# Optimization experiments

Hardware: AMD Instinct MI355X
Metric: run time of the kernel (lower is better)

Reference implementation:

```python
import jax, jax.numpy as jnp
import numpy as np

# static config (levels=4, CDA=False branch -> self_attn_4, scale=4, f=False)
SHAPES = [(80, 80), (40, 40), (20, 20), (10, 10)]
D = 256; NH = 8; NL = 4; NP = 4; DFF = 1024; DH = D // NH
L = sum(h * w for h, w in SHAPES)  # 8500
B = 1


def layer_norm(x, g, b, eps=1e-5):
    m = jnp.mean(x, axis=-1, keepdims=True)
    v = jnp.mean((x - m) ** 2, axis=-1, keepdims=True)
    return (x - m) * jax.lax.rsqrt(v + eps) * g + b


def ms_deform_attn_core(value, loc, attn):
    # value: [B, L, NH, DH]; loc: [B, Lq, NH, NL, NP, 2] in [0,1]; attn: [B, Lq, NH, NL, NP]
    Bq, Lq = loc.shape[0], loc.shape[1]
    out = jnp.zeros((Bq, NH, Lq, DH), value.dtype)
    start = 0
    for lvl, (Hl, Wl) in enumerate(SHAPES):
        v = value[:, start:start + Hl * Wl]          # [B, HW, NH, DH]
        start += Hl * Wl
        v = v.transpose(0, 2, 1, 3)                  # [B, NH, HW, DH]
        ll = loc[:, :, :, lvl]                       # [B, Lq, NH, NP, 2]
        # grid_sample semantics: align_corners=False, padding_mode='zeros'
        x = ll[..., 0] * Wl - 0.5
        y = ll[..., 1] * Hl - 0.5
        x0 = jnp.floor(x); y0 = jnp.floor(y)
        acc = jnp.zeros((Bq, NH, Lq, NP, DH), value.dtype)
        for dy in (0, 1):
            for dx in (0, 1):
                xi = x0 + dx; yi = y0 + dy
                w = (1.0 - jnp.abs(x - xi)) * (1.0 - jnp.abs(y - yi))  # [B,Lq,NH,NP]
                valid = (xi >= 0) & (xi < Wl) & (yi >= 0) & (yi < Hl)
                xi_c = jnp.clip(xi, 0, Wl - 1).astype(jnp.int32)
                yi_c = jnp.clip(yi, 0, Hl - 1).astype(jnp.int32)
                lin = (yi_c * Wl + xi_c).transpose(0, 2, 1, 3).reshape(Bq, NH, Lq * NP)
                g = jnp.take_along_axis(v, lin[..., None], axis=2).reshape(Bq, NH, Lq, NP, DH)
                wv = (w * valid.astype(w.dtype)).transpose(0, 2, 1, 3)[..., None]
                acc = acc + g * wv
        aw = attn[:, :, :, lvl].transpose(0, 2, 1, 3)[..., None]  # [B,NH,Lq,NP,1]
        out = out + jnp.sum(acc * aw, axis=3)
    return out.transpose(0, 2, 1, 3).reshape(Bq, Lq, NH * DH)


def setup_inputs():
    key = jax.random.key(0)
    ks = jax.random.split(key, 24)
    s = 0.02
    d = {}
    d['src'] = jax.random.normal(ks[0], (B, L, D), jnp.float32)
    d['pos'] = jax.random.normal(ks[1], (B, L, D), jnp.float32)
    d['reference_points'] = jax.random.uniform(ks[2], (B, L, NL, 2), jnp.float32)
    d['spatial_shapes'] = jnp.array(SHAPES, jnp.int32)
    d['level_start_index'] = jnp.array(np.cumsum([0] + [h * w for h, w in SHAPES[:-1]]), jnp.int32)
    d['scale'] = 4
    # MSDeformAttn params
    d['Wo'] = jax.random.normal(ks[3], (D, NH * NL * NP * 2), jnp.float32) * s
    d['bo'] = jax.random.normal(ks[4], (NH * NL * NP * 2,), jnp.float32) * s
    d['Wa'] = jax.random.normal(ks[5], (D, NH * NL * NP), jnp.float32) * s
    d['ba'] = jax.random.normal(ks[6], (NH * NL * NP,), jnp.float32) * s
    d['Wv'] = jax.random.normal(ks[7], (D, D), jnp.float32) * s
    d['bv'] = jnp.zeros((D,), jnp.float32)
    d['Wout'] = jax.random.normal(ks[8], (D, D), jnp.float32) * s
    d['bout'] = jnp.zeros((D,), jnp.float32)
    # FFN + LayerNorms
    d['W1'] = jax.random.normal(ks[9], (D, DFF), jnp.float32) * s
    d['b1'] = jnp.zeros((DFF,), jnp.float32)
    d['W2'] = jax.random.normal(ks[10], (DFF, D), jnp.float32) * s
    d['b2'] = jnp.zeros((D,), jnp.float32)
    d['g1'] = jnp.ones((D,), jnp.float32); d['be1'] = jnp.zeros((D,), jnp.float32)
    d['g2'] = jnp.ones((D,), jnp.float32); d['be2'] = jnp.zeros((D,), jnp.float32)
    return d


def reference(src, pos, reference_points, spatial_shapes, level_start_index, scale,
              Wo, bo, Wa, ba, Wv, bv, Wout, bout, W1, b1, W2, b2, g1, be1, g2, be2):
    Bq, Lq, _ = src.shape
    q = src + pos  # with_pos_embed
    # sampling offsets & attention weights (softmax over levels*points)
    off = (q @ Wo + bo).reshape(Bq, Lq, NH, NL, NP, 2)
    attn = jax.nn.softmax((q @ Wa + ba).reshape(Bq, Lq, NH, NL * NP), axis=-1)
    attn = attn.reshape(Bq, Lq, NH, NL, NP)
    value = (src @ Wv + bv).reshape(Bq, L, NH, DH)
    # offset normalizer is (W, H) per level
    normalizer = jnp.stack([spatial_shapes[:, 1], spatial_shapes[:, 0]], -1).astype(src.dtype)
    loc = reference_points[:, :, None, :, None, :] + off / normalizer[None, None, None, :, None, :]
    src2 = ms_deform_attn_core(value, loc, attn) @ Wout + bout
    # residual + norm1 (dropout = eval identity)
    x = layer_norm(src + src2, g1, be1)
    # FFN
    ffn = jax.nn.relu(x @ W1 + b1) @ W2 + b2
    x = layer_norm(x + ffn, g2, be2)
    return x
```

## Files before the change

### kernel.cpp

```cpp
#include <hip/hip_runtime.h>
#include <hip/hip_bf16.h>
#include <string.h>

#define D 256
#define NH 8
#define DH 32
#define NL 4
#define NP 4
#define DFF 1024
#define LTOT 8500

typedef __bf16 bf16x8 __attribute__((ext_vector_type(8)));
typedef float floatx4 __attribute__((ext_vector_type(4)));

__device__ inline unsigned bpack(float a, float b) {
    __hip_bfloat16 ha = __float2bfloat16(a), hb = __float2bfloat16(b);
    unsigned short ua, ub;
    memcpy(&ua, &ha, 2); memcpy(&ub, &hb, 2);
    return (unsigned)ua | ((unsigned)ub << 16);
}

__global__ void transpose_all(const float* W0, const float* W1_, const float* W2_,
                              const float* W3, const float* W4, const float* W5,
                              __hip_bfloat16* T0, __hip_bfloat16* T1, __hip_bfloat16* T2,
                              __hip_bfloat16* T3, __hip_bfloat16* T4, __hip_bfloat16* T5) {
    const int cum[7] = {0, 64, 96, 160, 224, 480, 736};
    int id = blockIdx.x;
    int mi = 0;
    while (id >= cum[mi + 1]) mi++;
    int lid = id - cum[mi];
    const float* W; __hip_bfloat16* T; int K, N;
    switch (mi) {
        case 0: W = W0; T = T0; K = 256;  N = 256;  break;
        case 1: W = W1_; T = T1; K = 256; N = 128;  break;
        case 2: W = W2_; T = T2; K = 256; N = 256;  break;
        case 3: W = W3; T = T3; K = 256;  N = 256;  break;
        case 4: W = W4; T = T4; K = 256;  N = 1024; break;
        default: W = W5; T = T5; K = 1024; N = 256; break;
    }
    int ntx = N >> 5;
    int n0 = (lid % ntx) * 32, k0 = (lid / ntx) * 32;
    __shared__ float t[32][33];
    int tx = threadIdx.x & 31, ty = threadIdx.x >> 5;
#pragma unroll
    for (int i = 0; i < 32; i += 8)
        t[ty + i][tx] = W[(size_t)(k0 + ty + i) * N + n0 + tx];
    __syncthreads();
#pragma unroll
    for (int i = 0; i < 32; i += 8)
        T[(size_t)(n0 + ty + i) * K + k0 + tx] = __float2bfloat16(t[tx][ty + i]);
}

template<int BM, int BN>
__global__ __launch_bounds__(256) void gemm_mfma(
    const __hip_bfloat16* __restrict__ A, const __hip_bfloat16* __restrict__ BT,
    const float* __restrict__ bias, float* __restrict__ Cf, __hip_bfloat16* __restrict__ Cb,
    int M, int N, int K, int relu) {
    constexpr int BK = 32;
    constexpr int LDA = BK + 8;
    __shared__ __align__(16) __hip_bfloat16 sA[BM * LDA];
    __shared__ __align__(16) __hip_bfloat16 sB[BN * LDA];

    int tid = threadIdx.x;
    int wave = tid >> 6, lane = tid & 63;
    int m0 = blockIdx.y * BM;
    int n0 = blockIdx.x * BN;
    constexpr int WM = BM / 2, WN = BN / 2;
    int wm = (wave >> 1) * WM;
    int wn = (wave & 1) * WN;
    constexpr int TM = WM / 16, TN = WN / 16;

    floatx4 acc[TM][TN];
#pragma unroll
    for (int i = 0; i < TM; i++)
#pragma unroll
        for (int j = 0; j < TN; j++)
#pragma unroll
            for (int e = 0; e < 4; e++) acc[i][j][e] = 0.f;

    constexpr int RA = BM / 64, RB = BN / 64;
    int rowT = tid >> 2;
    int c16 = tid & 3;
    int lrow = lane & 15;
    int lk = (lane >> 4) * 8;

    for (int k0 = 0; k0 < K; k0 += BK) {
#pragma unroll
        for (int r = 0; r < RA; r++) {
            int row = r * 64 + rowT;
            int grow = m0 + row; if (grow >= M) grow = M - 1;
            bf16x8 v = *(const bf16x8*)(A + (size_t)grow * K + k0 + c16 * 8);
            *(bf16x8*)(&sA[row * LDA + c16 * 8]) = v;
        }
#pragma unroll
        for (int r = 0; r < RB; r++) {
            int row = r * 64 + rowT;
            bf16x8 v = *(const bf16x8*)(BT + (size_t)(n0 + row) * K + k0 + c16 * 8);
            *(bf16x8*)(&sB[row * LDA + c16 * 8]) = v;
        }
        __syncthreads();

        bf16x8 af[TM], bfr[TN];
#pragma unroll
        for (int tm = 0; tm < TM; tm++)
            af[tm] = *(const bf16x8*)(&sA[(wm + tm * 16 + lrow) * LDA + lk]);
#pragma unroll
        for (int tn = 0; tn < TN; tn++)
            bfr[tn] = *(const bf16x8*)(&sB[(wn + tn * 16 + lrow) * LDA + lk]);
#pragma unroll
        for (int tm = 0; tm < TM; tm++)
#pragma unroll
            for (int tn = 0; tn < TN; tn++)
                acc[tm][tn] = __builtin_amdgcn_mfma_f32_16x16x32_bf16(af[tm], bfr[tn], acc[tm][tn], 0, 0, 0);
        __syncthreads();
    }

    int lcol = lane & 15;
    int lr4 = (lane >> 4) * 4;
#pragma unroll
    for (int tm = 0; tm < TM; tm++) {
#pragma unroll
        for (int i = 0; i < 4; i++) {
            int row = m0 + wm + tm * 16 + lr4 + i;
            if (row < M) {
#pragma unroll
                for (int tn = 0; tn < TN; tn++) {
                    int col = n0 + wn + tn * 16 + lcol;
                    float v = acc[tm][tn][i] + bias[col];
                    if (relu) v = fmaxf(v, 0.f);
                    if (Cf) Cf[(size_t)row * N + col] = v;
                    if (Cb) Cb[(size_t)row * N + col] = __float2bfloat16(v);
                }
            }
        }
    }
}

__global__ __launch_bounds__(256) void proj_fused(
    const float* __restrict__ src, const float* __restrict__ pos,
    const __hip_bfloat16* __restrict__ WoT, const __hip_bfloat16* __restrict__ WaT,
    const __hip_bfloat16* __restrict__ WvT,
    const float* __restrict__ bo, const float* __restrict__ ba, const float* __restrict__ bv,
    float* __restrict__ locb, float* __restrict__ attnb, __hip_bfloat16* __restrict__ valb,
    int M) {
    constexpr int BM = 64, BN = 64, BK = 32, K = 256;
    constexpr int LDA = BK + 8;
    __shared__ __align__(16) __hip_bfloat16 sA[BM * LDA];
    __shared__ __align__(16) __hip_bfloat16 sB[BN * LDA];

    int n0 = blockIdx.x * BN;
    int m0 = blockIdx.y * BM;

    const __hip_bfloat16* BT;
    const float* bias;
    int ncol0, Nout, usePos;
    float* Cf; __hip_bfloat16* Cb;
    if (n0 < 256)      { BT = WoT; bias = bo; ncol0 = n0;       Nout = 256; Cf = locb;  Cb = nullptr; usePos = 1; }
    else if (n0 < 384) { BT = WaT; bias = ba; ncol0 = n0 - 256; Nout = 128; Cf = attnb; Cb = nullptr; usePos = 1; }
    else               { BT = WvT; bias = bv; ncol0 = n0 - 384; Nout = 256; Cf = nullptr; Cb = valb; usePos = 0; }

    int tid = threadIdx.x;
    int wave = tid >> 6, lane = tid & 63;
    int wm = (wave >> 1) * 32;
    int wn = (wave & 1) * 32;

    floatx4 acc[2][2];
#pragma unroll
    for (int i = 0; i < 2; i++)
#pragma unroll
        for (int j = 0; j < 2; j++)
#pragma unroll
            for (int e = 0; e < 4; e++) acc[i][j][e] = 0.f;

    int rowT = tid >> 2, c16 = tid & 3;
    int lrow = lane & 15, lk = (lane >> 4) * 8;

    for (int k0 = 0; k0 < K; k0 += BK) {
        {
            int grow = m0 + rowT; if (grow >= M) grow = M - 1;
            const float* ap = src + (size_t)grow * K + k0 + c16 * 8;
            float4 s0 = *(const float4*)ap;
            float4 s1 = *(const float4*)(ap + 4);
            if (usePos) {
                const float* pp = pos + (size_t)grow * K + k0 + c16 * 8;
                float4 p0 = *(const float4*)pp;
                float4 p1 = *(const float4*)(pp + 4);
                s0.x += p0.x; s0.y += p0.y; s0.z += p0.z; s0.w += p0.w;
                s1.x += p1.x; s1.y += p1.y; s1.z += p1.z; s1.w += p1.w;
            }
            uint4 pk;
            pk.x = bpack(s0.x, s0.y); pk.y = bpack(s0.z, s0.w);
            pk.z = bpack(s1.x, s1.y); pk.w = bpack(s1.z, s1.w);
            *(uint4*)(&sA[rowT * LDA + c16 * 8]) = pk;
            *(bf16x8*)(&sB[rowT * LDA + c16 * 8]) =
                *(const bf16x8*)(BT + (size_t)(ncol0 + rowT) * K + k0 + c16 * 8);
        }
        __syncthreads();
        bf16x8 af[2], bfr[2];
#pragma unroll
        for (int t = 0; t < 2; t++) {
            af[t]  = *(const bf16x8*)(&sA[(wm + t * 16 + lrow) * LDA + lk]);
            bfr[t] = *(const bf16x8*)(&sB[(wn + t * 16 + lrow) * LDA + lk]);
        }
#pragma unroll
        for (int tm = 0; tm < 2; tm++)
#pragma unroll
            for (int tn = 0; tn < 2; tn++)
                acc[tm][tn] = __builtin_amdgcn_mfma_f32_16x16x32_bf16(af[tm], bfr[tn], acc[tm][tn], 0, 0, 0);
        __syncthreads();
    }

    int lcol = lane & 15, lr4 = (lane >> 4) * 4;
#pragma unroll
    for (int tm = 0; tm < 2; tm++) {
#pragma unroll
        for (int i = 0; i < 4; i++) {
            int row = m0 + wm + tm * 16 + lr4 + i;
            if (row < M) {
#pragma unroll
                for (int tn = 0; tn < 2; tn++) {
                    int col = ncol0 + wn + tn * 16 + lcol;
                    float v = acc[tm][tn][i] + bias[col];
                    if (Cf) Cf[(size_t)row * Nout + col] = v;
                    else    Cb[(size_t)row * Nout + col] = __float2bfloat16(v);
                }
            }
        }
    }
}

__global__ __launch_bounds__(256) void deform(const __hip_bfloat16* __restrict__ value,
                                              const float* __restrict__ locraw,
                                              const float* __restrict__ logits,
                                              const float* __restrict__ refp,
                                              __hip_bfloat16* __restrict__ out) {
    __shared__ float wS[4][8][16][4];
    __shared__ int   aS[4][8][16][4];
    int tid = threadIdx.x;
    int q0 = blockIdx.x * 4;

    {
        int sub = tid >> 6, h = (tid >> 3) & 7, t8 = tid & 7;
        int q = q0 + sub;
        const float* lg = logits + q * 128 + h * 16;
        float l0 = lg[t8], l1 = lg[t8 + 8];
        float mx = fmaxf(l0, l1);
#pragma unroll
        for (int m = 1; m < 8; m <<= 1) mx = fmaxf(mx, __shfl_xor(mx, m, 64));
        float e0 = __expf(l0 - mx), e1 = __expf(l1 - mx);
        float s = e0 + e1;
#pragma unroll
        for (int m = 1; m < 8; m <<= 1) s += __shfl_xor(s, m, 64);
        float inv = 1.f / s;

        const int starts[4] = {0, 6400, 8000, 8400};
#pragma unroll
        for (int j = 0; j < 2; j++) {
            int pp = t8 + 8 * j;
            float a = (j ? e1 : e0) * inv;
            int l = pp >> 2;
            int Wl = 80 >> l;
            float nv = (float)Wl;
            float rx = refp[q * 8 + l * 2 + 0];
            float ry = refp[q * 8 + l * 2 + 1];
            float lx = rx + locraw[q * 256 + h * 32 + pp * 2 + 0] / nv;
            float ly = ry + locraw[q * 256 + h * 32 + pp * 2 + 1] / nv;
            float x = lx * nv - 0.5f;
            float y = ly * nv - 0.5f;
            float x0f = floorf(x), y0f = floorf(y);
            float fx = x - x0f, fy = y - y0f;
            int x0 = (int)x0f, y0 = (int)y0f;
            float wts[4] = {(1.f - fx) * (1.f - fy), fx * (1.f - fy),
                            (1.f - fx) * fy,         fx * fy};
            int st = starts[l];
#pragma unroll
            for (int t = 0; t < 4; t++) {
                int xi = x0 + (t & 1), yi = y0 + (t >> 1);
                bool valid = (xi >= 0) & (xi < Wl) & (yi >= 0) & (yi < Wl);
                int xc = min(max(xi, 0), Wl - 1), yc = min(max(yi, 0), Wl - 1);
                wS[sub][h][pp][t] = valid ? wts[t] * a : 0.f;
                aS[sub][h][pp][t] = (st + yc * Wl + xc) * 512 + h * 64;
            }
        }
    }
    __syncthreads();

    int sub = tid >> 6, h = (tid >> 3) & 7, l8 = tid & 7;
    int q = q0 + sub;
    const char* vb = (const char*)value;
    int lo = l8 * 8;
    float a0 = 0.f, a1 = 0.f, a2 = 0.f, a3 = 0.f;
#pragma unroll
    for (int p = 0; p < 16; p++) {
        floatx4 w = *(const floatx4*)&wS[sub][h][p][0];
        int4 av = *(const int4*)&aS[sub][h][p][0];
#pragma unroll
        for (int t = 0; t < 4; t++) {
            int ad = (t == 0) ? av.x : (t == 1) ? av.y : (t == 2) ? av.z : av.w;
            uint2 u = *(const uint2*)(vb + ad + lo);
            float wt = w[t];
            a0 += wt * __uint_as_float(u.x << 16);
            a1 += wt * __uint_as_float(u.x & 0xffff0000u);
            a2 += wt * __uint_as_float(u.y << 16);
            a3 += wt * __uint_as_float(u.y & 0xffff0000u);
        }
    }
    uint2 o;
    o.x = bpack(a0, a1);
    o.y = bpack(a2, a3);
    *(uint2*)((char*)out + q * 512 + h * 64 + l8 * 8) = o;
}

__global__ __launch_bounds__(512) void gemm_ln(
    const __hip_bfloat16* __restrict__ A, const __hip_bfloat16* __restrict__ BT,
    const float* __restrict__ bias, const float* __restrict__ resid,
    const float* __restrict__ g, const float* __restrict__ be,
    float* __restrict__ outf, __hip_bfloat16* __restrict__ outb,
    int M, int K) {
    constexpr int BM = 32, BK = 32, LDA = BK + 8;
    __shared__ __align__(16) __hip_bfloat16 sA[BM * LDA];
    __shared__ __align__(16) __hip_bfloat16 sB[256 * LDA];
    __shared__ float psum[8][32], psq[8][32], mS[32], rS[32];

    int tid = threadIdx.x;
    int wave = tid >> 6, lane = tid & 63;
    int m0 = blockIdx.x * BM;

    floatx4 acc[2][2];
#pragma unroll
    for (int i = 0; i < 2; i++)
#pragma unroll
        for (int j = 0; j < 2; j++)
#pragma unroll
            for (int e = 0; e < 4; e++) acc[i][j][e] = 0.f;

    int rowT = tid >> 2, c16 = tid & 3;
    int lrow = lane & 15, lk = (lane >> 4) * 8;

    for (int k0 = 0; k0 < K; k0 += BK) {
        if (tid < 128) {
            int grow = m0 + rowT; if (grow >= M) grow = M - 1;
            *(bf16x8*)(&sA[rowT * LDA + c16 * 8]) =
                *(const bf16x8*)(A + (size_t)grow * K + k0 + c16 * 8);
        }
#pragma unroll
        for (int r = 0; r < 2; r++) {
            int row = r * 128 + rowT;
            *(bf16x8*)(&sB[row * LDA + c16 * 8]) =
                *(const bf16x8*)(BT + (size_t)row * K + k0 + c16 * 8);
        }
        __syncthreads();
        bf16x8 af[2], bfr[2];
#pragma unroll
        for (int tm = 0; tm < 2; tm++)
            af[tm] = *(const bf16x8*)(&sA[(tm * 16 + lrow) * LDA + lk]);
#pragma unroll
        for (int tn = 0; tn < 2; tn++)
            bfr[tn] = *(const bf16x8*)(&sB[(wave * 32 + tn * 16 + lrow) * LDA + lk]);
#pragma unroll
        for (int tm = 0; tm < 2; tm++)
#pragma unroll
            for (int tn = 0; tn < 2; tn++)
                acc[tm][tn] = __builtin_amdgcn_mfma_f32_16x16x32_bf16(af[tm], bfr[tn], acc[tm][tn], 0, 0, 0);
        __syncthreads();
    }

    int lcol = lane & 15, quad = lane >> 4;
    float v[2][2][4];
#pragma unroll
    for (int tm = 0; tm < 2; tm++) {
#pragma unroll
        for (int i = 0; i < 4; i++) {
            int row = tm * 16 + quad * 4 + i;
            int grow = m0 + row; if (grow >= M) grow = M - 1;
#pragma unroll
            for (int tn = 0; tn < 2; tn++) {
                int col = wave * 32 + tn * 16 + lcol;
                v[tm][tn][i] = acc[tm][tn][i] + bias[col] + resid[(size_t)grow * 256 + col];
            }
        }
    }

#pragma unroll
    for (int tm = 0; tm < 2; tm++) {
#pragma unroll
        for (int i = 0; i < 4; i++) {
            float s = 0.f, s2 = 0.f;
#pragma unroll
            for (int tn = 0; tn < 2; tn++) { float x = v[tm][tn][i]; s += x; s2 += x * x; }
#pragma unroll
            for (int m = 1; m < 16; m <<= 1) {
                s  += __shfl_xor(s, m, 64);
                s2 += __shfl_xor(s2, m, 64);
            }
            if (lcol == 0) {
                int row = tm * 16 + quad * 4 + i;
                psum[wave][row] = s;
                psq[wave][row]  = s2;
            }
        }
    }
    __syncthreads();
    if (tid < 32) {
        float s = 0.f, s2 = 0.f;
#pragma unroll
        for (int w = 0; w < 8; w++) { s += psum[w][tid]; s2 += psq[w][tid]; }
        float m = s * (1.f / 256.f);
        float var = fmaxf(s2 * (1.f / 256.f) - m * m, 0.f);
        mS[tid] = m;
        rS[tid] = rsqrtf(var + 1e-5f);
    }
    __syncthreads();

#pragma unroll
    for (int tm = 0; tm < 2; tm++) {
#pragma unroll
        for (int i = 0; i < 4; i++) {
            int row = tm * 16 + quad * 4 + i;
            int grow = m0 + row;
            if (grow < M) {
                float m = mS[row], r = rS[row];
#pragma unroll
                for (int tn = 0; tn < 2; tn++) {
                    int col = wave * 32 + tn * 16 + lcol;
                    float o = (v[tm][tn][i] - m) * r * g[col] + be[col];
                    outf[(size_t)grow * 256 + col] = o;
                    if (outb) outb[(size_t)grow * 256 + col] = __float2bfloat16(o);
                }
            }
        }
    }
}

extern "C" void kernel_launch(void* const* d_in, const int* in_sizes, int n_in,
                              void* d_out, int out_size, void* d_ws, size_t ws_size,
                              hipStream_t stream) {
    const float* src  = (const float*)d_in[0];
    const float* pos  = (const float*)d_in[1];
    const float* refp = (const float*)d_in[2];
    const float* Wo   = (const float*)d_in[6];
    const float* bo   = (const float*)d_in[7];
    const float* Wa   = (const float*)d_in[8];
    const float* ba   = (const float*)d_in[9];
    const float* Wv   = (const float*)d_in[10];
    const float* bv   = (const float*)d_in[11];
    const float* Wout = (const float*)d_in[12];
    const float* bout = (const float*)d_in[13];
    const float* W1   = (const float*)d_in[14];
    const float* b1   = (const float*)d_in[15];
    const float* W2   = (const float*)d_in[16];
    const float* b2   = (const float*)d_in[17];
    const float* g1   = (const float*)d_in[18];
    const float* be1  = (const float*)d_in[19];
    const float* g2   = (const float*)d_in[20];
    const float* be2  = (const float*)d_in[21];
    float* out = (float*)d_out;
    char* ws = (char*)d_ws;

    __hip_bfloat16* WoT   = (__hip_bfloat16*)(ws + 0);
    __hip_bfloat16* WaT   = (__hip_bfloat16*)(ws + 131072);
    __hip_bfloat16* WvT   = (__hip_bfloat16*)(ws + 196608);
    __hip_bfloat16* WoutT = (__hip_bfloat16*)(ws + 327680);
    __hip_bfloat16* W1T   = (__hip_bfloat16*)(ws + 458752);
    __hip_bfloat16* W2T   = (__hip_bfloat16*)(ws + 983040);
    float*          locb  = (float*)(ws + 1507328);
    float*          attnb = (float*)(ws + 10211328);
    __hip_bfloat16* valb  = (__hip_bfloat16*)(ws + 14563328);
    __hip_bfloat16* aob   = (__hip_bfloat16*)(ws + 18915328);
    float*          x1    = (float*)(ws + 23267328);
    __hip_bfloat16* x1b   = (__hip_bfloat16*)(ws + 31971328);
    __hip_bfloat16* hb    = (__hip_bfloat16*)(ws + 36323328);

    transpose_all<<<736, 256, 0, stream>>>(Wo, Wa, Wv, Wout, W1, W2,
                                           WoT, WaT, WvT, WoutT, W1T, W2T);

    proj_fused<<<dim3(10, 133), 256, 0, stream>>>(src, pos, WoT, WaT, WvT, bo, ba, bv,
                                                  locb, attnb, valb, LTOT);

    deform<<<2125, 256, 0, stream>>>(valb, locb, attnb, refp, aob);

    gemm_ln<<<266, 512, 0, stream>>>(aob, WoutT, bout, src, g1, be1, x1, x1b, LTOT, 256);
    gemm_mfma<128, 128><<<dim3(8, 67), 256, 0, stream>>>(x1b, W1T, b1, nullptr, hb, LTOT, 1024, 256, 1);
    gemm_ln<<<266, 512, 0, stream>>>(hb, W2T, b2, x1, g2, be2, out, nullptr, LTOT, 1024);
}
```

Before: 219.1 us.

## Fuse FFN GEMMs and LayerNorm into one kernel; widen projection tile

Replaces the separate W1 GEMM (writing the bf16 hidden activation to global memory) and the W2 GEMM+LayerNorm kernel with a single ffn_fused kernel. Each block handles 16 rows, keeps the 16x1024 hidden tile in shared memory and streams W1/W2 weights directly from global/L2. This removes the hidden-activation round trip and one launch, but reloads all FFN weights per 16-row block, which shifts pressure onto L2 bandwidth. Also doubles the projection kernel's N tile to 128, halving its grid and reusing each A tile across more columns.

Result: slower. 251.7 us (+14.9%).

```diff
diff --git a/kernel.cpp b/kernel.cpp
--- a/kernel.cpp
+++ b/kernel.cpp
@@ -51,91 +51,6 @@
         T[(size_t)(n0 + ty + i) * K + k0 + tx] = __float2bfloat16(t[tx][ty + i]);
 }
 
-template<int BM, int BN>
-__global__ __launch_bounds__(256) void gemm_mfma(
-    const __hip_bfloat16* __restrict__ A, const __hip_bfloat16* __restrict__ BT,
-    const float* __restrict__ bias, float* __restrict__ Cf, __hip_bfloat16* __restrict__ Cb,
-    int M, int N, int K, int relu) {
-    constexpr int BK = 32;
-    constexpr int LDA = BK + 8;
-    __shared__ __align__(16) __hip_bfloat16 sA[BM * LDA];
-    __shared__ __align__(16) __hip_bfloat16 sB[BN * LDA];
-
-    int tid = threadIdx.x;
-    int wave = tid >> 6, lane = tid & 63;
-    int m0 = blockIdx.y * BM;
-    int n0 = blockIdx.x * BN;
-    constexpr int WM = BM / 2, WN = BN / 2;
-    int wm = (wave >> 1) * WM;
-    int wn = (wave & 1) * WN;
-    constexpr int TM = WM / 16, TN = WN / 16;
-
-    floatx4 acc[TM][TN];
-#pragma unroll
-    for (int i = 0; i < TM; i++)
-#pragma unroll
-        for (int j = 0; j < TN; j++)
-#pragma unroll
-            for (int e = 0; e < 4; e++) acc[i][j][e] = 0.f;
-
-    constexpr int RA = BM / 64, RB = BN / 64;
-    int rowT = tid >> 2;
-    int c16 = tid & 3;
-    int lrow = lane & 15;
-    int lk = (lane >> 4) * 8;
-
-    for (int k0 = 0; k0 < K; k0 += BK) {
-#pragma unroll
-        for (int r = 0; r < RA; r++) {
-            int row = r * 64 + rowT;
-            int grow = m0 + row; if (grow >= M) grow = M - 1;
-            bf16x8 v = *(const bf16x8*)(A + (size_t)grow * K + k0 + c16 * 8);
-            *(bf16x8*)(&sA[row * LDA + c16 * 8]) = v;
-        }
-#pragma unroll
-        for (int r = 0; r < RB; r++) {
-            int row = r * 64 + rowT;
-            bf16x8 v = *(const bf16x8*)(BT + (size_t)(n0 + row) * K + k0 + c16 * 8);
-            *(bf16x8*)(&sB[row * LDA + c16 * 8]) = v;
-        }
-        __syncthreads();
-
-        bf16x8 af[TM], bfr[TN];
-#pragma unroll
-        for (int tm = 0; tm < TM; tm++)
-            af[tm] = *(const bf16x8*)(&sA[(wm + tm * 16 + lrow) * LDA + lk]);
-#pragma unroll
-        for (int tn = 0; tn < TN; tn++)
-            bfr[tn] = *(const bf16x8*)(&sB[(wn + tn * 16 + lrow) * LDA + lk]);
-#pragma unroll
-        for (int tm = 0; tm < TM; tm++)
-#pragma unroll
-            for (int tn = 0; tn < TN; tn++)
-                acc[tm][tn] = __builtin_amdgcn_mfma_f32_16x16x32_bf16(af[tm], bfr[tn], acc[tm][tn], 0, 0, 0);
-        __syncthreads();
-    }
-
-    int lcol = lane & 15;
-    int lr4 = (lane >> 4) * 4;
-#pragma unroll
-    for (int tm = 0; tm < TM; tm++) {
-#pragma unroll
-        for (int i = 0; i < 4; i++) {
-            int row = m0 + wm + tm * 16 + lr4 + i;
-            if (row < M) {
-#pragma unroll
-                for (int tn = 0; tn < TN; tn++) {
-                    int col = n0 + wn + tn * 16 + lcol;
-                    float v = acc[tm][tn][i] + bias[col];
-                    if (relu) v = fmaxf(v, 0.f);
-                    if (Cf) Cf[(size_t)row * N + col] = v;
-                    if (Cb) Cb[(size_t)row * N + col] = __float2bfloat16(v);
-                }
-            }
-        }
-    }
-}
-
 __global__ __launch_bounds__(256) void proj_fused(
     const float* __restrict__ src, const float* __restrict__ pos,
     const __hip_bfloat16* __restrict__ WoT, const __hip_bfloat16* __restrict__ WaT,
@@ -143,7 +58,7 @@
     const float* __restrict__ bo, const float* __restrict__ ba, const float* __restrict__ bv,
     float* __restrict__ locb, float* __restrict__ attnb, __hip_bfloat16* __restrict__ valb,
     int M) {
-    constexpr int BM = 64, BN = 64, BK = 32, K = 256;
+    constexpr int BM = 64, BN = 128, BK = 32, K = 256;
     constexpr int LDA = BK + 8;
     __shared__ __align__(16) __hip_bfloat16 sA[BM * LDA];
     __shared__ __align__(16) __hip_bfloat16 sB[BN * LDA];
@@ -162,13 +77,13 @@
     int tid = threadIdx.x;
     int wave = tid >> 6, lane = tid & 63;
     int wm = (wave >> 1) * 32;
-    int wn = (wave & 1) * 32;
-
-    floatx4 acc[2][2];
+    int wn = (wave & 1) * 64;
+
+    floatx4 acc[2][4];
 #pragma unroll
     for (int i = 0; i < 2; i++)
 #pragma unroll
-        for (int j = 0; j < 2; j++)
+        for (int j = 0; j < 4; j++)
 #pragma unroll
             for (int e = 0; e < 4; e++) acc[i][j][e] = 0.f;
 
@@ -192,20 +107,25 @@
             pk.x = bpack(s0.x, s0.y); pk.y = bpack(s0.z, s0.w);
             pk.z = bpack(s1.x, s1.y); pk.w = bpack(s1.z, s1.w);
             *(uint4*)(&sA[rowT * LDA + c16 * 8]) = pk;
-            *(bf16x8*)(&sB[rowT * LDA + c16 * 8]) =
-                *(const bf16x8*)(BT + (size_t)(ncol0 + rowT) * K + k0 + c16 * 8);
+#pragma unroll
+            for (int r = 0; r < 2; r++) {
+                int brow = r * 64 + rowT;
+                *(bf16x8*)(&sB[brow * LDA + c16 * 8]) =
+                    *(const bf16x8*)(BT + (size_t)(ncol0 + brow) * K + k0 + c16 * 8);
+            }
         }
         __syncthreads();
-        bf16x8 af[2], bfr[2];
-#pragma unroll
-        for (int t = 0; t < 2; t++) {
-            af[t]  = *(const bf16x8*)(&sA[(wm + t * 16 + lrow) * LDA + lk]);
+        bf16x8 af[2], bfr[4];
+#pragma unroll
+        for (int t = 0; t < 2; t++)
+            af[t] = *(const bf16x8*)(&sA[(wm + t * 16 + lrow) * LDA + lk]);
+#pragma unroll
+        for (int t = 0; t < 4; t++)
             bfr[t] = *(const bf16x8*)(&sB[(wn + t * 16 + lrow) * LDA + lk]);
-        }
 #pragma unroll
         for (int tm = 0; tm < 2; tm++)
 #pragma unroll
-            for (int tn = 0; tn < 2; tn++)
+            for (int tn = 0; tn < 4; tn++)
                 acc[tm][tn] = __builtin_amdgcn_mfma_f32_16x16x32_bf16(af[tm], bfr[tn], acc[tm][tn], 0, 0, 0);
         __syncthreads();
     }
@@ -218,7 +138,7 @@
             int row = m0 + wm + tm * 16 + lr4 + i;
             if (row < M) {
 #pragma unroll
-                for (int tn = 0; tn < 2; tn++) {
+                for (int tn = 0; tn < 4; tn++) {
                     int col = ncol0 + wn + tn * 16 + lcol;
                     float v = acc[tm][tn][i] + bias[col];
                     if (Cf) Cf[(size_t)row * Nout + col] = v;
@@ -427,6 +347,133 @@
                     outf[(size_t)grow * 256 + col] = o;
                     if (outb) outb[(size_t)grow * 256 + col] = __float2bfloat16(o);
                 }
+            }
+        }
+    }
+}
+
+__global__ __launch_bounds__(256) void ffn_fused(
+    const __hip_bfloat16* __restrict__ x1b, const float* __restrict__ x1,
+    const __hip_bfloat16* __restrict__ W1T, const float* __restrict__ b1,
+    const __hip_bfloat16* __restrict__ W2T, const float* __restrict__ b2,
+    const float* __restrict__ g, const float* __restrict__ be,
+    float* __restrict__ outf, int M) {
+    constexpr int LDH = 1048;
+    __shared__ __align__(16) __hip_bfloat16 sA[16 * 264];
+    __shared__ __align__(16) __hip_bfloat16 sH[16 * LDH];
+    __shared__ float psum[4][16], psq[4][16], mS[16], rS[16];
+
+    int tid = threadIdx.x;
+    int wave = tid >> 6, lane = tid & 63;
+    int m0 = blockIdx.x * 16;
+    int lrow = lane & 15, quad = lane >> 4;
+    int lk = quad * 8;
+
+    {
+        int ch = tid;
+#pragma unroll
+        for (int r = 0; r < 2; r++, ch += 256) {
+            int row = ch >> 5, col = (ch & 31) * 8;
+            int grow = m0 + row; if (grow >= M) grow = M - 1;
+            *(bf16x8*)(&sA[row * 264 + col]) = *(const bf16x8*)(x1b + (size_t)grow * 256 + col);
+        }
+    }
+    __syncthreads();
+
+#pragma unroll
+    for (int np = 0; np < 4; np++) {
+        int nbase = wave * 256 + np * 64;
+        floatx4 acc[4];
+#pragma unroll
+        for (int j = 0; j < 4; j++)
+#pragma unroll
+            for (int e = 0; e < 4; e++) acc[j][e] = 0.f;
+#pragma unroll
+        for (int k0 = 0; k0 < 256; k0 += 32) {
+            bf16x8 af = *(const bf16x8*)(&sA[lrow * 264 + k0 + lk]);
+#pragma unroll
+            for (int j = 0; j < 4; j++) {
+                bf16x8 bfb = *(const bf16x8*)(W1T + (size_t)(nbase + j * 16 + lrow) * 256 + k0 + lk);
+                acc[j] = __builtin_amdgcn_mfma_f32_16x16x32_bf16(af, bfb, acc[j], 0, 0, 0);
+            }
+        }
+#pragma unroll
+        for (int j = 0; j < 4; j++) {
+            int col = nbase + j * 16 + lrow;
+            float bb = b1[col];
+#pragma unroll
+            for (int i = 0; i < 4; i++) {
+                int row = quad * 4 + i;
+                float hv = fmaxf(acc[j][i] + bb, 0.f);
+                sH[row * LDH + col] = __float2bfloat16(hv);
+            }
+        }
+    }
+    __syncthreads();
+
+    floatx4 acc2[4];
+#pragma unroll
+    for (int j = 0; j < 4; j++)
+#pragma unroll
+        for (int e = 0; e < 4; e++) acc2[j][e] = 0.f;
+    for (int k0 = 0; k0 < 1024; k0 += 32) {
+        bf16x8 af = *(const bf16x8*)(&sH[lrow * LDH + k0 + lk]);
+#pragma unroll
+        for (int j = 0; j < 4; j++) {
+            bf16x8 bfb = *(const bf16x8*)(W2T + (size_t)(wave * 64 + j * 16 + lrow) * 1024 + k0 + lk);
+            acc2[j] = __builtin_amdgcn_mfma_f32_16x16x32_bf16(af, bfb, acc2[j], 0, 0, 0);
+        }
+    }
+
+    float v[4][4];
+#pragma unroll
+    for (int j = 0; j < 4; j++) {
+        int col = wave * 64 + j * 16 + lrow;
+        float bb = b2[col];
+#pragma unroll
+        for (int i = 0; i < 4; i++) {
+            int row = quad * 4 + i;
+            int grow = m0 + row; if (grow >= M) grow = M - 1;
+            v[j][i] = acc2[j][i] + bb + x1[(size_t)grow * 256 + col];
+        }
+    }
+#pragma unroll
+    for (int i = 0; i < 4; i++) {
+        float s = 0.f, s2 = 0.f;
+#pragma unroll
+        for (int j = 0; j < 4; j++) { float x = v[j][i]; s += x; s2 += x * x; }
+#pragma unroll
+        for (int m = 1; m < 16; m <<= 1) {
+            s  += __shfl_xor(s, m, 64);
+            s2 += __shfl_xor(s2, m, 64);
+        }
+        if (lrow == 0) {
+            int row = quad * 4 + i;
+            psum[wave][row] = s;
+            psq[wave][row]  = s2;
+        }
+    }
+    __syncthreads();
+    if (tid < 16) {
+        float s = 0.f, s2 = 0.f;
+#pragma unroll
+        for (int w = 0; w < 4; w++) { s += psum[w][tid]; s2 += psq[w][tid]; }
+        float m = s * (1.f / 256.f);
+        float var = fmaxf(s2 * (1.f / 256.f) - m * m, 0.f);
+        mS[tid] = m;
+        rS[tid] = rsqrtf(var + 1e-5f);
+    }
+    __syncthreads();
+#pragma unroll
+    for (int i = 0; i < 4; i++) {
+        int row = quad * 4 + i;
+        int grow = m0 + row;
+        if (grow < M) {
+            float m = mS[row], r = rS[row];
+#pragma unroll
+            for (int j = 0; j < 4; j++) {
+                int col = wave * 64 + j * 16 + lrow;
+                outf[(size_t)grow * 256 + col] = (v[j][i] - m) * r * g[col] + be[col];
             }
         }
     }
@@ -469,17 +516,16 @@
     __hip_bfloat16* aob   = (__hip_bfloat16*)(ws + 18915328);
     float*          x1    = (float*)(ws + 23267328);
     __hip_bfloat16* x1b   = (__hip_bfloat16*)(ws + 31971328);
-    __hip_bfloat16* hb    = (__hip_bfloat16*)(ws + 36323328);
 
     transpose_all<<<736, 256, 0, stream>>>(Wo, Wa, Wv, Wout, W1, W2,
                                            WoT, WaT, WvT, WoutT, W1T, W2T);
 
-    proj_fused<<<dim3(10, 133), 256, 0, stream>>>(src, pos, WoT, WaT, WvT, bo, ba, bv,
-                                                  locb, attnb, valb, LTOT);
+    proj_fused<<<dim3(5, 133), 256, 0, stream>>>(src, pos, WoT, WaT, WvT, bo, ba, bv,
+                                                 locb, attnb, valb, LTOT);
 
     deform<<<2125, 256, 0, stream>>>(valb, locb, attnb, refp, aob);
 
     gemm_ln<<<266, 512, 0, stream>>>(aob, WoutT, bout, src, g1, be1, x1, x1b, LTOT, 256);
-    gemm_mfma<128, 128><<<dim3(8, 67), 256, 0, stream>>>(x1b, W1T, b1, nullptr, hb, LTOT, 1024, 256, 1);
-    gemm_ln<<<266, 512, 0, stream>>>(hb, W2T, b2, x1, g2, be2, out, nullptr, LTOT, 1024);
-}
+
+    ffn_fused<<<532, 256, 0, stream>>>(x1b, x1, W1T, b1, W2T, b2, g2, be2, out, LTOT);
+}
```

## Prefetch next K-tile into registers in GEMM kernels; widen proj tile N

Applied to the files above, without the earlier changes.

In the generic GEMM, the fused projection and the GEMM+LayerNorm kernels, the global loads for the next K-slice are now issued into registers right after the barrier. They are stored to shared memory at the start of the next iteration, so global-memory latency overlaps with the MFMA work on the current tile. The fused projection kernel also doubles its N tile to 128, halving the grid in x and reusing each A tile across more output columns. This raises register pressure, which may lower occupancy.

New measurement: 209.6 us. -4.3%, faster.

```diff
diff --git a/kernel.cpp b/kernel.cpp
--- a/kernel.cpp
+++ b/kernel.cpp
@@ -84,21 +84,39 @@
     int lrow = lane & 15;
     int lk = (lane >> 4) * 8;
 
+    int growA[RA];
+#pragma unroll
+    for (int r = 0; r < RA; r++) {
+        int g = m0 + r * 64 + rowT; if (g >= M) g = M - 1;
+        growA[r] = g;
+    }
+
+    bf16x8 pa[RA], pb[RB];
+#pragma unroll
+    for (int r = 0; r < RA; r++)
+        pa[r] = *(const bf16x8*)(A + (size_t)growA[r] * K + c16 * 8);
+#pragma unroll
+    for (int r = 0; r < RB; r++)
+        pb[r] = *(const bf16x8*)(BT + (size_t)(n0 + r * 64 + rowT) * K + c16 * 8);
+
     for (int k0 = 0; k0 < K; k0 += BK) {
 #pragma unroll
-        for (int r = 0; r < RA; r++) {
-            int row = r * 64 + rowT;
-            int grow = m0 + row; if (grow >= M) grow = M - 1;
-            bf16x8 v = *(const bf16x8*)(A + (size_t)grow * K + k0 + c16 * 8);
-            *(bf16x8*)(&sA[row * LDA + c16 * 8]) = v;
-        }
-#pragma unroll
-        for (int r = 0; r < RB; r++) {
-            int row = r * 64 + rowT;
-            bf16x8 v = *(const bf16x8*)(BT + (size_t)(n0 + row) * K + k0 + c16 * 8);
-            *(bf16x8*)(&sB[row * LDA + c16 * 8]) = v;
-        }
+        for (int r = 0; r < RA; r++)
+            *(bf16x8*)(&sA[(r * 64 + rowT) * LDA + c16 * 8]) = pa[r];
+#pragma unroll
+        for (int r = 0; r < RB; r++)
+            *(bf16x8*)(&sB[(r * 64 + rowT) * LDA + c16 * 8]) = pb[r];
         __syncthreads();
+
+        int kn = k0 + BK;
+        if (kn < K) {
+#pragma unroll
+            for (int r = 0; r < RA; r++)
+                pa[r] = *(const bf16x8*)(A + (size_t)growA[r] * K + kn + c16 * 8);
+#pragma unroll
+            for (int r = 0; r < RB; r++)
+                pb[r] = *(const bf16x8*)(BT + (size_t)(n0 + r * 64 + rowT) * K + kn + c16 * 8);
+        }
 
         bf16x8 af[TM], bfr[TN];
 #pragma unroll
@@ -143,7 +161,7 @@
     const float* __restrict__ bo, const float* __restrict__ ba, const float* __restrict__ bv,
     float* __restrict__ locb, float* __restrict__ attnb, __hip_bfloat16* __restrict__ valb,
     int M) {
-    constexpr int BM = 64, BN = 64, BK = 32, K = 256;
+    constexpr int BM = 64, BN = 128, BK = 32, K = 256;
     constexpr int LDA = BK + 8;
     __shared__ __align__(16) __hip_bfloat16 sA[BM * LDA];
     __shared__ __align__(16) __hip_bfloat16 sB[BN * LDA];
@@ -162,50 +180,75 @@
     int tid = threadIdx.x;
     int wave = tid >> 6, lane = tid & 63;
     int wm = (wave >> 1) * 32;
-    int wn = (wave & 1) * 32;
-
-    floatx4 acc[2][2];
+    int wn = (wave & 1) * 64;
+
+    floatx4 acc[2][4];
 #pragma unroll
     for (int i = 0; i < 2; i++)
 #pragma unroll
-        for (int j = 0; j < 2; j++)
+        for (int j = 0; j < 4; j++)
 #pragma unroll
             for (int e = 0; e < 4; e++) acc[i][j][e] = 0.f;
 
     int rowT = tid >> 2, c16 = tid & 3;
     int lrow = lane & 15, lk = (lane >> 4) * 8;
 
+    int growA = m0 + rowT; if (growA >= M) growA = M - 1;
+    const float* aBase = src + (size_t)growA * K + c16 * 8;
+    const float* pBase = pos + (size_t)growA * K + c16 * 8;
+
+    float4 s0, s1, p0, p1;
+    bf16x8 pb[2];
+    {
+        s0 = *(const float4*)aBase;
+        s1 = *(const float4*)(aBase + 4);
+        if (usePos) { p0 = *(const float4*)pBase; p1 = *(const float4*)(pBase + 4); }
+#pragma unroll
+        for (int r = 0; r < 2; r++)
+            pb[r] = *(const bf16x8*)(BT + (size_t)(ncol0 + r * 64 + rowT) * K + c16 * 8);
+    }
+
     for (int k0 = 0; k0 < K; k0 += BK) {
         {
-            int grow = m0 + rowT; if (grow >= M) grow = M - 1;
-            const float* ap = src + (size_t)grow * K + k0 + c16 * 8;
-            float4 s0 = *(const float4*)ap;
-            float4 s1 = *(const float4*)(ap + 4);
+            float4 a0 = s0, a1 = s1;
             if (usePos) {
-                const float* pp = pos + (size_t)grow * K + k0 + c16 * 8;
-                float4 p0 = *(const float4*)pp;
-                float4 p1 = *(const float4*)(pp + 4);
-                s0.x += p0.x; s0.y += p0.y; s0.z += p0.z; s0.w += p0.w;
-                s1.x += p1.x; s1.y += p1.y; s1.z += p1.z; s1.w += p1.w;
+                a0.x += p0.x; a0.y += p0.y; a0.z += p0.z; a0.w += p0.w;
+                a1.x += p1.x; a1.y += p1.y; a1.z += p1.z; a1.w += p1.w;
             }
             uint4 pk;
-            pk.x = bpack(s0.x, s0.y); pk.y = bpack(s0.z, s0.w);
-            pk.z = bpack(s1.x, s1.y); pk.w = bpack(s1.z, s1.w);
+            pk.x = bpack(a0.x, a0.y); pk.y = bpack(a0.z, a0.w);
+            pk.z = bpack(a1.x, a1.y); pk.w = bpack(a1.z, a1.w);
             *(uint4*)(&sA[rowT * LDA + c16 * 8]) = pk;
-            *(bf16x8*)(&sB[rowT * LDA + c16 * 8]) =
-                *(const bf16x8*)(BT + (size_t)(ncol0 + rowT) * K + k0 + c16 * 8);
+#pragma unroll
+            for (int r = 0; r < 2; r++)
+                *(bf16x8*)(&sB[(r * 64 + rowT) * LDA + c16 * 8]) = pb[r];
         }
         __syncthreads();
-        bf16x8 af[2], bfr[2];
-#pragma unroll
-        for (int t = 0; t < 2; t++) {
-            af[t]  = *(const bf16x8*)(&sA[(wm + t * 16 + lrow) * LDA + lk]);
+
+        int kn = k0 + BK;
+        if (kn < K) {
+            s0 = *(const float4*)(aBase + kn);
+            s1 = *(const float4*)(aBase + kn + 4);
+            if (usePos) {
+                p0 = *(const float4*)(pBase + kn);
+                p1 = *(const float4*)(pBase + kn + 4);
+            }
+#pragma unroll
+            for (int r = 0; r < 2; r++)
+                pb[r] = *(const bf16x8*)(BT + (size_t)(ncol0 + r * 64 + rowT) * K + kn + c16 * 8);
+        }
+
+        bf16x8 af[2], bfr[4];
+#pragma unroll
+        for (int t = 0; t < 2; t++)
+            af[t] = *(const bf16x8*)(&sA[(wm + t * 16 + lrow) * LDA + lk]);
+#pragma unroll
+        for (int t = 0; t < 4; t++)
             bfr[t] = *(const bf16x8*)(&sB[(wn + t * 16 + lrow) * LDA + lk]);
-        }
 #pragma unroll
         for (int tm = 0; tm < 2; tm++)
 #pragma unroll
-            for (int tn = 0; tn < 2; tn++)
+            for (int tn = 0; tn < 4; tn++)
                 acc[tm][tn] = __builtin_amdgcn_mfma_f32_16x16x32_bf16(af[tm], bfr[tn], acc[tm][tn], 0, 0, 0);
         __syncthreads();
     }
@@ -218,7 +261,7 @@
             int row = m0 + wm + tm * 16 + lr4 + i;
             if (row < M) {
 #pragma unroll
-                for (int tn = 0; tn < 2; tn++) {
+                for (int tn = 0; tn < 4; tn++) {
                     int col = ncol0 + wn + tn * 16 + lcol;
                     float v = acc[tm][tn][i] + bias[col];
                     if (Cf) Cf[(size_t)row * Nout + col] = v;
@@ -337,19 +380,32 @@
     int rowT = tid >> 2, c16 = tid & 3;
     int lrow = lane & 15, lk = (lane >> 4) * 8;
 
+    int growA = m0 + rowT; if (growA >= M) growA = M - 1;
+
+    bf16x8 pA, pB[2];
+    if (tid < 128)
+        pA = *(const bf16x8*)(A + (size_t)growA * K + c16 * 8);
+#pragma unroll
+    for (int r = 0; r < 2; r++)
+        pB[r] = *(const bf16x8*)(BT + (size_t)(r * 128 + rowT) * K + c16 * 8);
+
     for (int k0 = 0; k0 < K; k0 += BK) {
-        if (tid < 128) {
-            int grow = m0 + rowT; if (grow >= M) grow = M - 1;
-            *(bf16x8*)(&sA[rowT * LDA + c16 * 8]) =
-                *(const bf16x8*)(A + (size_t)grow * K + k0 + c16 * 8);
-        }
-#pragma unroll
-        for (int r = 0; r < 2; r++) {
-            int row = r * 128 + rowT;
-            *(bf16x8*)(&sB[row * LDA + c16 * 8]) =
-                *(const bf16x8*)(BT + (size_t)row * K + k0 + c16 * 8);
-        }
+        if (tid < 128)
+            *(bf16x8*)(&sA[rowT * LDA + c16 * 8]) = pA;
+#pragma unroll
+        for (int r = 0; r < 2; r++)
+            *(bf16x8*)(&sB[(r * 128 + rowT) * LDA + c16 * 8]) = pB[r];
         __syncthreads();
+
+        int kn = k0 + BK;
+        if (kn < K) {
+            if (tid < 128)
+                pA = *(const bf16x8*)(A + (size_t)growA * K + kn + c16 * 8);
+#pragma unroll
+            for (int r = 0; r < 2; r++)
+                pB[r] = *(const bf16x8*)(BT + (size_t)(r * 128 + rowT) * K + kn + c16 * 8);
+        }
+
         bf16x8 af[2], bfr[2];
 #pragma unroll
         for (int tm = 0; tm < 2; tm++)
@@ -474,12 +530,14 @@
     transpose_all<<<736, 256, 0, stream>>>(Wo, Wa, Wv, Wout, W1, W2,
                                            WoT, WaT, WvT, WoutT, W1T, W2T);
 
-    proj_fused<<<dim3(10, 133), 256, 0, stream>>>(src, pos, WoT, WaT, WvT, bo, ba, bv,
-                                                  locb, attnb, valb, LTOT);
+    proj_fused<<<dim3(5, 133), 256, 0, stream>>>(src, pos, WoT, WaT, WvT, bo, ba, bv,
+                                                 locb, attnb, valb, LTOT);
 
     deform<<<2125, 256, 0, stream>>>(valb, locb, attnb, refp, aob);
 
     gemm_ln<<<266, 512, 0, stream>>>(aob, WoutT, bout, src, g1, be1, x1, x1b, LTOT, 256);
+
     gemm_mfma<128, 128><<<dim3(8, 67), 256, 0, stream>>>(x1b, W1T, b1, nullptr, hb, LTOT, 1024, 256, 1);
+
     gemm_ln<<<266, 512, 0, stream>>>(hb, W2T, b2, x1, g2, be2, out, nullptr, LTOT, 1024);
 }
```
